# Kernel optimization log

Hardware: AMD Instinct MI355X
Metric: run time of the kernel (lower is better)

## Reference

```python
import jax, jax.numpy as jnp
import numpy as np

B, S, H, L = 8, 4096, 768, 256   # batch, seq_len, hidden_size, num_lines (= line_ids.max()+1)
ATT_HID = 1024                    # attention MLP hidden dim from nn.Linear(hidden,1024)


def setup_inputs() -> dict:
    key = jax.random.key(0)
    k0, k1, k2, k3 = jax.random.split(key, 4)
    token_hidden = jax.random.normal(k0, (B, S, H), dtype=jnp.float32)
    line_ids = jax.random.randint(k1, (B, S), 0, L)  # all valid; -1 would mark invalid
    W1 = jax.random.normal(k2, (H, ATT_HID), dtype=jnp.float32) * 0.02
    b1 = jnp.zeros((ATT_HID,), jnp.float32)
    W2 = jax.random.normal(k3, (ATT_HID, 1), dtype=jnp.float32) * 0.02
    b2 = jnp.zeros((1,), jnp.float32)
    return {"token_hidden": token_hidden, "line_ids": line_ids,
            "W1": W1, "b1": b1, "W2": W2, "b2": b2}


def reference(token_hidden, line_ids, W1, b1, W2, b2):
    b, s, h = token_hidden.shape
    num_lines = L
    n_seg = b * num_lines + 1  # last segment is a dump slot for invalid (-1) tokens

    # attention scores: Linear -> tanh -> Linear, squeeze(-1)  [b, s]
    scores = (jnp.tanh(token_hidden @ W1 + b1) @ W2 + b2)[..., 0]

    valid = (line_ids >= 0).reshape(-1)                                   # [b*s]
    seg = jnp.where(line_ids >= 0,
                    jnp.arange(b)[:, None] * num_lines + line_ids,
                    b * num_lines).reshape(-1)                            # [b*s]
    s_flat = jnp.where(valid, scores.reshape(-1), -jnp.inf)

    # segment-wise stable softmax
    m = jax.ops.segment_max(s_flat, seg, num_segments=n_seg)
    m = jnp.where(jnp.isfinite(m), m, 0.0)  # empty segments -> safe 0
    e = jnp.where(valid, jnp.exp(scores.reshape(-1) - m[seg]), 0.0)
    denom = jax.ops.segment_sum(e, seg, num_segments=n_seg)
    w = e / jnp.maximum(denom[seg], 1e-20)                                # [b*s]

    # weighted sum of tokens per (batch, line) segment
    feats = jax.ops.segment_sum(token_hidden.reshape(-1, h) * w[:, None],
                                seg, num_segments=n_seg)
    line_features = feats[: b * num_lines].reshape(b, num_lines, h)

    counts = jax.ops.segment_sum(valid.astype(jnp.float32), seg, num_segments=n_seg)
    line_mask = counts[: b * num_lines].reshape(b, num_lines) > 0
    return line_features, line_mask
```

## Files before the change

kernel.cpp:

```cpp
#include <hip/hip_runtime.h>
#include <hip/hip_bf16.h>
#include <string.h>

#define M_TOK 32768
#define H_DIM 768
#define AH    1024
#define NSEG  2048
#define LCAP  192
#define NKT   12
#define CONV_BLK 1024

typedef __attribute__((ext_vector_type(8))) __bf16 bf16x8;
typedef __attribute__((ext_vector_type(4))) float f32x4;

__device__ __forceinline__ float tanh_fast(float x) {
  float e = __expf(2.0f * x);
  return 1.0f - 2.0f * __builtin_amdgcn_rcpf(e + 1.0f);
}

__device__ __forceinline__ float bf2f(unsigned short u) {
  unsigned int v = (unsigned int)u << 16;
  float f;
  memcpy(&f, &v, 4);
  return f;
}

__global__ __launch_bounds__(256) void prep_kernel(
    const float* __restrict__ W1, __hip_bfloat16* __restrict__ W1t,
    const float4* __restrict__ X4, uint4* __restrict__ Xb4) {
  __shared__ float tile[32][33];
  if (blockIdx.x < 768) {
    int nt = blockIdx.x & 31, ktile = blockIdx.x >> 5;
    int n0 = nt * 32, k0 = ktile * 32;
    int tx = threadIdx.x & 31, ty = threadIdx.x >> 5;
    for (int r = ty; r < 32; r += 8)
      tile[r][tx] = W1[(size_t)(k0 + r) * AH + n0 + tx];
    __syncthreads();
    for (int r = ty; r < 32; r += 8)
      W1t[(size_t)(n0 + r) * H_DIM + k0 + tx] = __float2bfloat16(tile[tx][r]);
  } else {
    const int i0 = (blockIdx.x - 768) * (256 * 12) + threadIdx.x;
#pragma unroll
    for (int p = 0; p < 12; ++p) {
      const size_t i = (size_t)i0 + p * 256;
      float4 v0 = X4[i * 2];
      float4 v1 = X4[i * 2 + 1];
      __hip_bfloat16 h[8] = {
          __float2bfloat16(v0.x), __float2bfloat16(v0.y),
          __float2bfloat16(v0.z), __float2bfloat16(v0.w),
          __float2bfloat16(v1.x), __float2bfloat16(v1.y),
          __float2bfloat16(v1.z), __float2bfloat16(v1.w)};
      uint4 pk;
      memcpy(&pk, h, 16);
      Xb4[i] = pk;
    }
  }
}

#define WAITV(N) asm volatile("s_waitcnt vmcnt(" #N ")" ::: "memory")
#define WAITL0   asm volatile("s_waitcnt lgkmcnt(0)" ::: "memory")

__global__ __launch_bounds__(512, 2) void attn_score_kernel(
    const __hip_bfloat16* __restrict__ Xbg,
    const __hip_bfloat16* __restrict__ W1tg, const float* __restrict__ b1g,
    const float* __restrict__ W2g, float* __restrict__ scores2) {
  __shared__ __align__(16) __bf16 As[2][256 * 64];
  __shared__ __align__(16) __bf16 Bs[2][256 * 64];

  const int tid = threadIdx.x;
  const int bid = blockIdx.x;
  const int xcd = bid & 7;
  const int sq  = bid >> 3;
  const int m0  = (xcd * 16 + (sq >> 1)) * 256;
  const int np0 = (sq & 1) * 512;
  const int lane = tid & 63;
  const int wave = tid >> 6;
  const int wm   = wave >> 2;
  const int wx   = wave & 3;
  const int ml   = lane & 15;
  const int lh   = lane >> 4;

  const __bf16* Xb = (const __bf16*)Xbg;
  const __bf16* W  = (const __bf16*)W1tg;

  const int lr   = tid >> 3;
  const int scol = ((tid & 7) ^ (lr & 7)) << 3;

  int aRow[4], bRow[4];
#pragma unroll
  for (int q = 0; q < 4; ++q) {
    aRow[q] = m0 + ((q & 1) << 7) + ((q >> 1) << 6) + lr;
    int lrow = (q << 6) + lr;
    bRow[q] = np0 + (((lrow >> 5) & 3) << 6) + ((lrow >> 7) << 5) + (lrow & 31);
  }

  f32x4 acc[8][4];
#pragma unroll
  for (int i = 0; i < 8; ++i)
#pragma unroll
    for (int j = 0; j < 4; ++j) acc[i][j] = (f32x4)0.f;

  bf16x8 af[4][2], bfr[2][2];

  float b1v[2][4], w2v[2][4];
#pragma unroll
  for (int sd = 0; sd < 2; ++sd)
#pragma unroll
    for (int nf = 0; nf < 4; ++nf) {
      int n = np0 + sd * 256 + wx * 64 + nf * 16 + ml;
      b1v[sd][nf] = b1g[n];
      w2v[sd][nf] = W2g[n];
    }
  WAITV(0);

#define STAGE_A(q, buf, kt)                                                    \
  __builtin_amdgcn_global_load_lds(                                            \
      (const __attribute__((address_space(1))) void*)(Xb +                     \
          (size_t)aRow[q] * H_DIM + (kt) + scol),                              \
      (__attribute__((address_space(3))) void*)&As[buf][(q) * 4096 + tid * 8], \
      16, 0, 0)
#define STAGE_B(q, buf, kt, nsh)                                               \
  __builtin_amdgcn_global_load_lds(                                            \
      (const __attribute__((address_space(1))) void*)(W +                      \
          (size_t)(bRow[q] + (nsh)) * H_DIM + (kt) + scol),                    \
      (__attribute__((address_space(3))) void*)&Bs[buf][(q) * 4096 + tid * 8], \
      16, 0, 0)

#define DSRA(MH, P)                                                            \
  _Pragma("unroll") for (int lf = 0; lf < 4; ++lf) {                           \
    int ra = ((MH) << 7) + (wm << 6) + (lf << 4) + ml;                         \
    _Pragma("unroll") for (int kk = 0; kk < 2; ++kk) {                         \
      int ph = ((kk << 2) + lh) ^ (ml & 7);                                    \
      af[lf][kk] = *(const bf16x8*)&As[P][(ra << 6) + (ph << 3)];              \
    }                                                                          \
  }
#define DSRB(NH, P)                                                            \
  _Pragma("unroll") for (int jj = 0; jj < 2; ++jj) {                           \
    int rb = ((NH) << 7) + (wx << 5) + (jj << 4) + ml;                         \
    _Pragma("unroll") for (int kk = 0; kk < 2; ++kk) {                         \
      int ph = ((kk << 2) + lh) ^ (ml & 7);                                    \
      bfr[jj][kk] = *(const bf16x8*)&Bs[P][(rb << 6) + (ph << 3)];             \
    }                                                                          \
  }
#define MFMAQ(MH, NH)                                                          \
  __builtin_amdgcn_s_setprio(1);                                               \
  _Pragma("unroll") for (int kk = 0; kk < 2; ++kk)                             \
    _Pragma("unroll") for (int lf = 0; lf < 4; ++lf)                           \
      _Pragma("unroll") for (int jj = 0; jj < 2; ++jj)                         \
        acc[(MH) * 4 + lf][(NH) * 2 + jj] =                                    \
            __builtin_amdgcn_mfma_f32_16x16x32_bf16(                           \
                af[lf][kk], bfr[jj][kk], acc[(MH) * 4 + lf][(NH) * 2 + jj],    \
                0, 0, 0);                                                      \
  __builtin_amdgcn_s_setprio(0);

#define BARRIER __builtin_amdgcn_s_barrier()
#define SCHED0  __builtin_amdgcn_sched_barrier(0)

#define EPILOGUE(side)                                                         \
  {                                                                            \
    __syncthreads();                                                           \
    float* red = (float*)&As[1][0];                                            \
    _Pragma("unroll") for (int mf = 0; mf < 8; ++mf) {                         \
      _Pragma("unroll") for (int pp = 0; pp < 4; ++pp) {                       \
        float tsum = 0.f;                                                      \
        _Pragma("unroll") for (int nf = 0; nf < 4; ++nf)                       \
          tsum += tanh_fast(acc[mf][nf][pp] + b1v[side][nf]) * w2v[side][nf];  \
        tsum += __shfl_xor(tsum, 1);                                           \
        tsum += __shfl_xor(tsum, 2);                                           \
        tsum += __shfl_xor(tsum, 4);                                           \
        tsum += __shfl_xor(tsum, 8);                                           \
        if (ml == 0)                                                           \
          red[wx * 256 + wm * 128 + mf * 16 + lh * 4 + pp] = tsum;             \
      }                                                                        \
    }                                                                          \
    __syncthreads();                                                           \
    if (tid < 256) {                                                           \
      float v =                                                                \
          (red[tid] + red[256 + tid]) + (red[512 + tid] + red[768 + tid]);     \
      scores2[(size_t)(m0 + tid) * 4 + ((sq & 1) * 2 + (side))] = v;           \
    }                                                                          \
  }

  STAGE_A(0, 0, 0); STAGE_A(1, 0, 0);
  STAGE_B(0, 0, 0, 0); STAGE_B(1, 0, 0, 0);
  STAGE_A(2, 0, 0); STAGE_A(3, 0, 0);
  STAGE_B(2, 0, 0, 0); STAGE_B(3, 0, 0, 0);
  WAITV(4);
  BARRIER;

  int P = 0;
  for (int tt = 0; tt < 2 * NKT - 1; ++tt) {
    const int u   = tt + 1;
    const int ktu = ((u >= NKT) ? (u - NKT) : u) << 6;
    const int nsh = (u >= NKT) ? 256 : 0;

    DSRA(0, P); DSRB(0, P);
    STAGE_A(0, P ^ 1, ktu); STAGE_A(1, P ^ 1, ktu);
    asm volatile("s_waitcnt lgkmcnt(8)" ::: "memory");
    BARRIER;
    WAITL0; SCHED0;
    MFMAQ(0, 0);
    WAITV(4);
    BARRIER;

    DSRA(1, P);
    STAGE_B(0, P ^ 1, ktu, nsh); STAGE_B(1, P ^ 1, ktu, nsh);
    BARRIER;
    WAITL0; SCHED0;
    MFMAQ(1, 0);
    WAITV(4);
    BARRIER;

    DSRB(1, P);
    STAGE_A(2, P ^ 1, ktu); STAGE_A(3, P ^ 1, ktu);
    BARRIER;
    WAITL0; SCHED0;
    MFMAQ(1, 1);
    BARRIER;

    DSRA(0, P);
    STAGE_B(2, P ^ 1, ktu, nsh); STAGE_B(3, P ^ 1, ktu, nsh);
    BARRIER;
    WAITL0; SCHED0;
    MFMAQ(0, 1);
    WAITV(4);
    BARRIER;

    P ^= 1;

    if (tt == NKT - 1) {
      EPILOGUE(0);
#pragma unroll
      for (int i = 0; i < 8; ++i)
#pragma unroll
        for (int j = 0; j < 4; ++j) acc[i][j] = (f32x4)0.f;
      WAITV(0);
      __syncthreads();
    }
  }

  DSRA(0, 1); DSRB(0, 1);
  asm volatile("s_waitcnt lgkmcnt(8)" ::: "memory");
  BARRIER;
  WAITL0; SCHED0;
  MFMAQ(0, 0);
  WAITV(2);
  BARRIER;

  DSRA(1, 1);
  BARRIER;
  WAITL0; SCHED0;
  MFMAQ(1, 0);
  WAITV(0);
  BARRIER;

  DSRB(1, 1);
  BARRIER;
  WAITL0; SCHED0;
  MFMAQ(1, 1);
  BARRIER;

  DSRA(0, 1);
  BARRIER;
  WAITL0; SCHED0;
  MFMAQ(0, 1);

  EPILOGUE(1);
}

__global__ __launch_bounds__(256) void aggregate_kernel(
    const ushort* __restrict__ Xb, const float* __restrict__ scores2,
    const int* __restrict__ line_ids, float4* __restrict__ out4,
    float* __restrict__ out_mask) {
  __shared__ int   slist[LCAP];
  __shared__ float sw[LCAP];
  __shared__ float wred[4];
  __shared__ int   cnt_sh;
  const int seg = blockIdx.x;
  const int b = seg >> 8, lid = seg & 255;
  const int tid = threadIdx.x, lane = tid & 63, wave = tid >> 6;
  const int base = b * 4096;

  if (tid == 0) cnt_sh = 0;

  int ids[16];
#pragma unroll
  for (int c = 0; c < 16; ++c) ids[c] = line_ids[base + c * 256 + tid];
  __syncthreads();

#pragma unroll
  for (int c = 0; c < 16; ++c) {
    bool match = (ids[c] == lid);
    unsigned long long mask = __ballot(match);
    int cw = __popcll(mask);
    int bpos = 0;
    if (lane == 0 && cw) bpos = atomicAdd(&cnt_sh, cw);
    bpos = __shfl(bpos, 0);
    if (match) {
      int pos = bpos + __popcll(mask & ((1ull << lane) - 1ull));
      if (pos < LCAP) slist[pos] = base + c * 256 + tid;
    }
  }
  __syncthreads();
  int total = cnt_sh;
  int cnt = total > LCAP ? LCAP : total;
  if (tid == 0) out_mask[seg] = cnt > 0 ? 1.f : 0.f;
  if (cnt == 0) {
    if (tid < H_DIM / 4)
      out4[(size_t)seg * (H_DIM / 4) + tid] = make_float4(0.f, 0.f, 0.f, 0.f);
    return;
  }
  float lmax = -3.4e38f;
  if (tid < cnt) {
    const float4 a = *(const float4*)(scores2 + (size_t)slist[tid] * 4);
    float sc = (a.x + a.y) + (a.z + a.w);
    sw[tid] = sc;
    lmax = sc;
  }
#pragma unroll
  for (int d = 1; d < 64; d <<= 1) lmax = fmaxf(lmax, __shfl_xor(lmax, d));
  if (lane == 0) wred[wave] = lmax;
  __syncthreads();
  float m = fmaxf(fmaxf(wred[0], wred[1]), fmaxf(wred[2], wred[3]));
  float lsum = 0.f;
  if (tid < cnt) {
    float e = __expf(sw[tid] - m);
    sw[tid] = e;
    lsum = e;
  }
#pragma unroll
  for (int d = 1; d < 64; d <<= 1) lsum += __shfl_xor(lsum, d);
  __syncthreads();
  if (lane == 0) wred[wave] = lsum;
  __syncthreads();
  float denom = wred[0] + wred[1] + wred[2] + wred[3];
  float inv = __builtin_amdgcn_rcpf(fmaxf(denom, 1e-20f));
  if (tid < cnt) sw[tid] *= inv;
  __syncthreads();
  if (tid < H_DIM / 4) {
    const ushort4* xb = (const ushort4*)Xb + tid;
    float4 acc = make_float4(0.f, 0.f, 0.f, 0.f);
    int t = 0;
    for (; t + 4 <= cnt; t += 4) {
      ushort4 u0 = xb[(size_t)slist[t]     * (H_DIM / 4)];
      ushort4 u1 = xb[(size_t)slist[t + 1] * (H_DIM / 4)];
      ushort4 u2 = xb[(size_t)slist[t + 2] * (H_DIM / 4)];
      ushort4 u3 = xb[(size_t)slist[t + 3] * (H_DIM / 4)];
      float w0 = sw[t], w1 = sw[t + 1], w2 = sw[t + 2], w3 = sw[t + 3];
      acc.x += w0 * bf2f(u0.x) + w1 * bf2f(u1.x) + w2 * bf2f(u2.x) + w3 * bf2f(u3.x);
      acc.y += w0 * bf2f(u0.y) + w1 * bf2f(u1.y) + w2 * bf2f(u2.y) + w3 * bf2f(u3.y);
      acc.z += w0 * bf2f(u0.z) + w1 * bf2f(u1.z) + w2 * bf2f(u2.z) + w3 * bf2f(u3.z);
      acc.w += w0 * bf2f(u0.w) + w1 * bf2f(u1.w) + w2 * bf2f(u2.w) + w3 * bf2f(u3.w);
    }
    for (; t < cnt; ++t) {
      ushort4 u = xb[(size_t)slist[t] * (H_DIM / 4)];
      float w = sw[t];
      acc.x += w * bf2f(u.x); acc.y += w * bf2f(u.y);
      acc.z += w * bf2f(u.z); acc.w += w * bf2f(u.w);
    }
    out4[(size_t)seg * (H_DIM / 4) + tid] = acc;
  }
}

extern "C" void kernel_launch(void* const* d_in, const int* in_sizes, int n_in,
                              void* d_out, int out_size, void* d_ws, size_t ws_size,
                              hipStream_t stream) {
  const float* X        = (const float*)d_in[0];
  const int*   line_ids = (const int*)d_in[1];
  const float* W1       = (const float*)d_in[2];
  const float* b1       = (const float*)d_in[3];
  const float* W2       = (const float*)d_in[4];

  char* p = (char*)d_ws;
  __hip_bfloat16* Xb      = (__hip_bfloat16*)p;  p += (size_t)M_TOK * H_DIM * 2;
  __hip_bfloat16* W1t     = (__hip_bfloat16*)p;  p += 1572864;
  float*          scores2 = (float*)p;           p += (size_t)M_TOK * 4 * 4;

  float* out_feats = (float*)d_out;
  float* out_mask  = out_feats + (size_t)NSEG * H_DIM;

  prep_kernel<<<768 + CONV_BLK, 256, 0, stream>>>(
      W1, W1t, (const float4*)X, (uint4*)Xb);
  attn_score_kernel<<<256, 512, 0, stream>>>(Xb, W1t, b1, W2, scores2);
  aggregate_kernel<<<NSEG, 256, 0, stream>>>((const ushort*)Xb, scores2,
                                             line_ids, (float4*)out_feats,
                                             out_mask);
}
```

Measured before the change: 236.7 us.

## Fuse X fp32-to-bf16 conversion into GEMM A-tile loads, aggregate from fp32 X

Removes the separate X conversion pass and the bf16 copy of X. The GEMM now loads fp32 X through registers, converts it to bf16 and writes it into LDS, replacing direct global-to-LDS loads, with the load and wait schedule reworked. The aggregate kernel reads fp32 X directly. This saves a full read and write pass over X, but doubles the bytes read for the A operand and for the gather, and adds register pressure and VALU conversion work inside the GEMM pipeline.

New measurement: 253.0 us. 1.07x slower.

```diff
diff --git a/kernel.cpp b/kernel.cpp
--- a/kernel.cpp
+++ b/kernel.cpp
@@ -8,7 +8,6 @@
 #define NSEG  2048
 #define LCAP  192
 #define NKT   12
-#define CONV_BLK 1024
 
 typedef __attribute__((ext_vector_type(8))) __bf16 bf16x8;
 typedef __attribute__((ext_vector_type(4))) float f32x4;
@@ -18,50 +17,24 @@
   return 1.0f - 2.0f * __builtin_amdgcn_rcpf(e + 1.0f);
 }
 
-__device__ __forceinline__ float bf2f(unsigned short u) {
-  unsigned int v = (unsigned int)u << 16;
-  float f;
-  memcpy(&f, &v, 4);
-  return f;
-}
-
 __global__ __launch_bounds__(256) void prep_kernel(
-    const float* __restrict__ W1, __hip_bfloat16* __restrict__ W1t,
-    const float4* __restrict__ X4, uint4* __restrict__ Xb4) {
+    const float* __restrict__ W1, __hip_bfloat16* __restrict__ W1t) {
   __shared__ float tile[32][33];
-  if (blockIdx.x < 768) {
-    int nt = blockIdx.x & 31, ktile = blockIdx.x >> 5;
-    int n0 = nt * 32, k0 = ktile * 32;
-    int tx = threadIdx.x & 31, ty = threadIdx.x >> 5;
-    for (int r = ty; r < 32; r += 8)
-      tile[r][tx] = W1[(size_t)(k0 + r) * AH + n0 + tx];
-    __syncthreads();
-    for (int r = ty; r < 32; r += 8)
-      W1t[(size_t)(n0 + r) * H_DIM + k0 + tx] = __float2bfloat16(tile[tx][r]);
-  } else {
-    const int i0 = (blockIdx.x - 768) * (256 * 12) + threadIdx.x;
-#pragma unroll
-    for (int p = 0; p < 12; ++p) {
-      const size_t i = (size_t)i0 + p * 256;
-      float4 v0 = X4[i * 2];
-      float4 v1 = X4[i * 2 + 1];
-      __hip_bfloat16 h[8] = {
-          __float2bfloat16(v0.x), __float2bfloat16(v0.y),
-          __float2bfloat16(v0.z), __float2bfloat16(v0.w),
-          __float2bfloat16(v1.x), __float2bfloat16(v1.y),
-          __float2bfloat16(v1.z), __float2bfloat16(v1.w)};
-      uint4 pk;
-      memcpy(&pk, h, 16);
-      Xb4[i] = pk;
-    }
-  }
+  int nt = blockIdx.x & 31, ktile = blockIdx.x >> 5;
+  int n0 = nt * 32, k0 = ktile * 32;
+  int tx = threadIdx.x & 31, ty = threadIdx.x >> 5;
+  for (int r = ty; r < 32; r += 8)
+    tile[r][tx] = W1[(size_t)(k0 + r) * AH + n0 + tx];
+  __syncthreads();
+  for (int r = ty; r < 32; r += 8)
+    W1t[(size_t)(n0 + r) * H_DIM + k0 + tx] = __float2bfloat16(tile[tx][r]);
 }
 
 #define WAITV(N) asm volatile("s_waitcnt vmcnt(" #N ")" ::: "memory")
 #define WAITL0   asm volatile("s_waitcnt lgkmcnt(0)" ::: "memory")
 
 __global__ __launch_bounds__(512, 2) void attn_score_kernel(
-    const __hip_bfloat16* __restrict__ Xbg,
+    const float* __restrict__ Xf,
     const __hip_bfloat16* __restrict__ W1tg, const float* __restrict__ b1g,
     const float* __restrict__ W2g, float* __restrict__ scores2) {
   __shared__ __align__(16) __bf16 As[2][256 * 64];
@@ -80,7 +53,6 @@
   const int ml   = lane & 15;
   const int lh   = lane >> 4;
 
-  const __bf16* Xb = (const __bf16*)Xbg;
   const __bf16* W  = (const __bf16*)W1tg;
 
   const int lr   = tid >> 3;
@@ -101,6 +73,7 @@
     for (int j = 0; j < 4; ++j) acc[i][j] = (f32x4)0.f;
 
   bf16x8 af[4][2], bfr[2][2];
+  float4 ald[4][2];
 
   float b1v[2][4], w2v[2][4];
 #pragma unroll
@@ -113,12 +86,25 @@
     }
   WAITV(0);
 
-#define STAGE_A(q, buf, kt)                                                    \
-  __builtin_amdgcn_global_load_lds(                                            \
-      (const __attribute__((address_space(1))) void*)(Xb +                     \
-          (size_t)aRow[q] * H_DIM + (kt) + scol),                              \
-      (__attribute__((address_space(3))) void*)&As[buf][(q) * 4096 + tid * 8], \
-      16, 0, 0)
+#define LOAD_A(q, kt)                                                          \
+  {                                                                            \
+    const float* ga = Xf + (size_t)aRow[q] * H_DIM + (kt) + scol;              \
+    ald[q][0] = *(const float4*)ga;                                            \
+    ald[q][1] = *(const float4*)(ga + 4);                                      \
+  }
+#define WRITE_A(q, buf)                                                        \
+  {                                                                            \
+    union { bf16x8 v; __hip_bfloat16 h[8]; } u_;                               \
+    u_.h[0] = __float2bfloat16(ald[q][0].x);                                   \
+    u_.h[1] = __float2bfloat16(ald[q][0].y);                                   \
+    u_.h[2] = __float2bfloat16(ald[q][0].z);                                   \
+    u_.h[3] = __float2bfloat16(ald[q][0].w);                                   \
+    u_.h[4] = __float2bfloat16(ald[q][1].x);                                   \
+    u_.h[5] = __float2bfloat16(ald[q][1].y);                                   \
+    u_.h[6] = __float2bfloat16(ald[q][1].z);                                   \
+    u_.h[7] = __float2bfloat16(ald[q][1].w);                                   \
+    *(bf16x8*)&As[buf][(q) * 4096 + tid * 8] = u_.v;                           \
+  }
 #define STAGE_B(q, buf, kt, nsh)                                               \
   __builtin_amdgcn_global_load_lds(                                            \
       (const __attribute__((address_space(1))) void*)(W +                      \
@@ -181,11 +167,13 @@
     }                                                                          \
   }
 
-  STAGE_A(0, 0, 0); STAGE_A(1, 0, 0);
+  LOAD_A(0, 0); LOAD_A(1, 0); LOAD_A(2, 0); LOAD_A(3, 0);
   STAGE_B(0, 0, 0, 0); STAGE_B(1, 0, 0, 0);
-  STAGE_A(2, 0, 0); STAGE_A(3, 0, 0);
   STAGE_B(2, 0, 0, 0); STAGE_B(3, 0, 0, 0);
   WAITV(4);
+  WRITE_A(0, 0); WRITE_A(1, 0); WRITE_A(2, 0); WRITE_A(3, 0);
+  WAITV(0);
+  WAITL0;
   BARRIER;
 
   int P = 0;
@@ -195,35 +183,35 @@
     const int nsh = (u >= NKT) ? 256 : 0;
 
     DSRA(0, P); DSRB(0, P);
-    STAGE_A(0, P ^ 1, ktu); STAGE_A(1, P ^ 1, ktu);
+    LOAD_A(0, ktu); LOAD_A(1, ktu); LOAD_A(2, ktu); LOAD_A(3, ktu);
+    STAGE_B(0, P ^ 1, ktu, nsh); STAGE_B(1, P ^ 1, ktu, nsh);
+    STAGE_B(2, P ^ 1, ktu, nsh); STAGE_B(3, P ^ 1, ktu, nsh);
     asm volatile("s_waitcnt lgkmcnt(8)" ::: "memory");
     BARRIER;
     WAITL0; SCHED0;
     MFMAQ(0, 0);
-    WAITV(4);
     BARRIER;
 
     DSRA(1, P);
-    STAGE_B(0, P ^ 1, ktu, nsh); STAGE_B(1, P ^ 1, ktu, nsh);
     BARRIER;
     WAITL0; SCHED0;
     MFMAQ(1, 0);
+    BARRIER;
+
+    DSRB(1, P);
     WAITV(4);
-    BARRIER;
-
-    DSRB(1, P);
-    STAGE_A(2, P ^ 1, ktu); STAGE_A(3, P ^ 1, ktu);
+    WRITE_A(0, P ^ 1); WRITE_A(1, P ^ 1);
+    WRITE_A(2, P ^ 1); WRITE_A(3, P ^ 1);
     BARRIER;
     WAITL0; SCHED0;
     MFMAQ(1, 1);
     BARRIER;
 
     DSRA(0, P);
-    STAGE_B(2, P ^ 1, ktu, nsh); STAGE_B(3, P ^ 1, ktu, nsh);
     BARRIER;
     WAITL0; SCHED0;
     MFMAQ(0, 1);
-    WAITV(4);
+    WAITV(0);
     BARRIER;
 
     P ^= 1;
@@ -244,14 +232,12 @@
   BARRIER;
   WAITL0; SCHED0;
   MFMAQ(0, 0);
-  WAITV(2);
   BARRIER;
 
   DSRA(1, 1);
   BARRIER;
   WAITL0; SCHED0;
   MFMAQ(1, 0);
-  WAITV(0);
   BARRIER;
 
   DSRB(1, 1);
@@ -269,7 +255,7 @@
 }
 
 __global__ __launch_bounds__(256) void aggregate_kernel(
-    const ushort* __restrict__ Xb, const float* __restrict__ scores2,
+    const float* __restrict__ Xf, const float* __restrict__ scores2,
     const int* __restrict__ line_ids, float4* __restrict__ out4,
     float* __restrict__ out_mask) {
   __shared__ int   slist[LCAP];
@@ -338,25 +324,25 @@
   if (tid < cnt) sw[tid] *= inv;
   __syncthreads();
   if (tid < H_DIM / 4) {
-    const ushort4* xb = (const ushort4*)Xb + tid;
+    const float4* xb = (const float4*)Xf + tid;
     float4 acc = make_float4(0.f, 0.f, 0.f, 0.f);
     int t = 0;
     for (; t + 4 <= cnt; t += 4) {
-      ushort4 u0 = xb[(size_t)slist[t]     * (H_DIM / 4)];
-      ushort4 u1 = xb[(size_t)slist[t + 1] * (H_DIM / 4)];
-      ushort4 u2 = xb[(size_t)slist[t + 2] * (H_DIM / 4)];
-      ushort4 u3 = xb[(size_t)slist[t + 3] * (H_DIM / 4)];
+      float4 u0 = xb[(size_t)slist[t]     * (H_DIM / 4)];
+      float4 u1 = xb[(size_t)slist[t + 1] * (H_DIM / 4)];
+      float4 u2 = xb[(size_t)slist[t + 2] * (H_DIM / 4)];
+      float4 u3 = xb[(size_t)slist[t + 3] * (H_DIM / 4)];
       float w0 = sw[t], w1 = sw[t + 1], w2 = sw[t + 2], w3 = sw[t + 3];
-      acc.x += w0 * bf2f(u0.x) + w1 * bf2f(u1.x) + w2 * bf2f(u2.x) + w3 * bf2f(u3.x);
-      acc.y += w0 * bf2f(u0.y) + w1 * bf2f(u1.y) + w2 * bf2f(u2.y) + w3 * bf2f(u3.y);
-      acc.z += w0 * bf2f(u0.z) + w1 * bf2f(u1.z) + w2 * bf2f(u2.z) + w3 * bf2f(u3.z);
-      acc.w += w0 * bf2f(u0.w) + w1 * bf2f(u1.w) + w2 * bf2f(u2.w) + w3 * bf2f(u3.w);
+      acc.x += w0 * u0.x + w1 * u1.x + w2 * u2.x + w3 * u3.x;
+      acc.y += w0 * u0.y + w1 * u1.y + w2 * u2.y + w3 * u3.y;
+      acc.z += w0 * u0.z + w1 * u1.z + w2 * u2.z + w3 * u3.z;
+      acc.w += w0 * u0.w + w1 * u1.w + w2 * u2.w + w3 * u3.w;
     }
     for (; t < cnt; ++t) {
-      ushort4 u = xb[(size_t)slist[t] * (H_DIM / 4)];
+      float4 u = xb[(size_t)slist[t] * (H_DIM / 4)];
       float w = sw[t];
-      acc.x += w * bf2f(u.x); acc.y += w * bf2f(u.y);
-      acc.z += w * bf2f(u.z); acc.w += w * bf2f(u.w);
+      acc.x += w * u.x; acc.y += w * u.y;
+      acc.z += w * u.z; acc.w += w * u.w;
     }
     out4[(size_t)seg * (H_DIM / 4) + tid] = acc;
   }
@@ -372,17 +358,14 @@
   const float* W2       = (const float*)d_in[4];
 
   char* p = (char*)d_ws;
-  __hip_bfloat16* Xb      = (__hip_bfloat16*)p;  p += (size_t)M_TOK * H_DIM * 2;
   __hip_bfloat16* W1t     = (__hip_bfloat16*)p;  p += 1572864;
   float*          scores2 = (float*)p;           p += (size_t)M_TOK * 4 * 4;
 
   float* out_feats = (float*)d_out;
   float* out_mask  = out_feats + (size_t)NSEG * H_DIM;
 
-  prep_kernel<<<768 + CONV_BLK, 256, 0, stream>>>(
-      W1, W1t, (const float4*)X, (uint4*)Xb);
-  attn_score_kernel<<<256, 512, 0, stream>>>(Xb, W1t, b1, W2, scores2);
-  aggregate_kernel<<<NSEG, 256, 0, stream>>>((const ushort*)Xb, scores2,
-                                             line_ids, (float4*)out_feats,
-                                             out_mask);
-}
+  prep_kernel<<<768, 256, 0, stream>>>(W1, W1t);
+  attn_score_kernel<<<256, 512, 0, stream>>>(X, W1t, b1, W2, scores2);
+  aggregate_kernel<<<NSEG, 256, 0, stream>>>(X, scores2, line_ids,
+                                             (float4*)out_feats, out_mask);
+}
```

## Fuse score GEMM and segment aggregation into one cooperative kernel with grid sync

Applied to the files above, without the earlier changes.

Merges the attention-score GEMM kernel and the per-segment softmax/weighted-sum kernel into a single cooperative launch of 256 blocks, separated by a grid-wide sync. After the sync each block handles 8 segments, reusing the GEMM's shared memory for its token list and weights, and splits the weighted accumulation across two thread groups. This removes one kernel launch and the gap between the two kernels. The cost is that aggregation now runs on only 256 blocks instead of 2048, which lowers parallelism for that phase, and the grid sync itself adds overhead.

After: 351.6 us. 48.6% more time.

```diff
diff --git a/kernel.cpp b/kernel.cpp
--- a/kernel.cpp
+++ b/kernel.cpp
@@ -1,6 +1,9 @@
 #include <hip/hip_runtime.h>
 #include <hip/hip_bf16.h>
+#include <hip/hip_cooperative_groups.h>
 #include <string.h>
+
+namespace cg = cooperative_groups;
 
 #define M_TOK 32768
 #define H_DIM 768
@@ -8,7 +11,6 @@
 #define NSEG  2048
 #define LCAP  192
 #define NKT   12
-#define CONV_BLK 1024
 
 typedef __attribute__((ext_vector_type(8))) __bf16 bf16x8;
 typedef __attribute__((ext_vector_type(4))) float f32x4;
@@ -60,10 +62,12 @@
 #define WAITV(N) asm volatile("s_waitcnt vmcnt(" #N ")" ::: "memory")
 #define WAITL0   asm volatile("s_waitcnt lgkmcnt(0)" ::: "memory")
 
-__global__ __launch_bounds__(512, 2) void attn_score_kernel(
+__global__ __launch_bounds__(512, 2) void fused_kernel(
     const __hip_bfloat16* __restrict__ Xbg,
     const __hip_bfloat16* __restrict__ W1tg, const float* __restrict__ b1g,
-    const float* __restrict__ W2g, float* __restrict__ scores2) {
+    const float* __restrict__ W2g, float* __restrict__ scores2,
+    const int* __restrict__ line_ids, float4* __restrict__ out4,
+    float* __restrict__ out_mask) {
   __shared__ __align__(16) __bf16 As[2][256 * 64];
   __shared__ __align__(16) __bf16 Bs[2][256 * 64];
 
@@ -266,99 +270,109 @@
   MFMAQ(0, 1);
 
   EPILOGUE(1);
-}
-
-__global__ __launch_bounds__(256) void aggregate_kernel(
-    const ushort* __restrict__ Xb, const float* __restrict__ scores2,
-    const int* __restrict__ line_ids, float4* __restrict__ out4,
-    float* __restrict__ out_mask) {
-  __shared__ int   slist[LCAP];
-  __shared__ float sw[LCAP];
-  __shared__ float wred[4];
-  __shared__ int   cnt_sh;
-  const int seg = blockIdx.x;
-  const int b = seg >> 8, lid = seg & 255;
-  const int tid = threadIdx.x, lane = tid & 63, wave = tid >> 6;
+
+  __threadfence();
+  cg::this_grid().sync();
+
+  float4* gredL = (float4*)&As[0][0];
+  int*    slist = (int*)(gredL + 192);
+  float*  sw    = (float*)(slist + 192);
+  float*  wredf = sw + 192;
+  int*    cntp  = (int*)(wredf + 8);
+
+  const int segbase = bid * 8;
+  const int b    = segbase >> 8;
   const int base = b * 4096;
 
-  if (tid == 0) cnt_sh = 0;
-
-  int ids[16];
-#pragma unroll
-  for (int c = 0; c < 16; ++c) ids[c] = line_ids[base + c * 256 + tid];
-  __syncthreads();
-
-#pragma unroll
-  for (int c = 0; c < 16; ++c) {
-    bool match = (ids[c] == lid);
-    unsigned long long mask = __ballot(match);
-    int cw = __popcll(mask);
-    int bpos = 0;
-    if (lane == 0 && cw) bpos = atomicAdd(&cnt_sh, cw);
-    bpos = __shfl(bpos, 0);
-    if (match) {
-      int pos = bpos + __popcll(mask & ((1ull << lane) - 1ull));
-      if (pos < LCAP) slist[pos] = base + c * 256 + tid;
-    }
-  }
-  __syncthreads();
-  int total = cnt_sh;
-  int cnt = total > LCAP ? LCAP : total;
-  if (tid == 0) out_mask[seg] = cnt > 0 ? 1.f : 0.f;
-  if (cnt == 0) {
-    if (tid < H_DIM / 4)
-      out4[(size_t)seg * (H_DIM / 4) + tid] = make_float4(0.f, 0.f, 0.f, 0.f);
-    return;
-  }
-  float lmax = -3.4e38f;
-  if (tid < cnt) {
-    const float4 a = *(const float4*)(scores2 + (size_t)slist[tid] * 4);
-    float sc = (a.x + a.y) + (a.z + a.w);
-    sw[tid] = sc;
-    lmax = sc;
-  }
-#pragma unroll
-  for (int d = 1; d < 64; d <<= 1) lmax = fmaxf(lmax, __shfl_xor(lmax, d));
-  if (lane == 0) wred[wave] = lmax;
-  __syncthreads();
-  float m = fmaxf(fmaxf(wred[0], wred[1]), fmaxf(wred[2], wred[3]));
-  float lsum = 0.f;
-  if (tid < cnt) {
-    float e = __expf(sw[tid] - m);
-    sw[tid] = e;
-    lsum = e;
-  }
-#pragma unroll
-  for (int d = 1; d < 64; d <<= 1) lsum += __shfl_xor(lsum, d);
-  __syncthreads();
-  if (lane == 0) wred[wave] = lsum;
-  __syncthreads();
-  float denom = wred[0] + wred[1] + wred[2] + wred[3];
-  float inv = __builtin_amdgcn_rcpf(fmaxf(denom, 1e-20f));
-  if (tid < cnt) sw[tid] *= inv;
-  __syncthreads();
-  if (tid < H_DIM / 4) {
-    const ushort4* xb = (const ushort4*)Xb + tid;
-    float4 acc = make_float4(0.f, 0.f, 0.f, 0.f);
-    int t = 0;
-    for (; t + 4 <= cnt; t += 4) {
-      ushort4 u0 = xb[(size_t)slist[t]     * (H_DIM / 4)];
-      ushort4 u1 = xb[(size_t)slist[t + 1] * (H_DIM / 4)];
-      ushort4 u2 = xb[(size_t)slist[t + 2] * (H_DIM / 4)];
-      ushort4 u3 = xb[(size_t)slist[t + 3] * (H_DIM / 4)];
-      float w0 = sw[t], w1 = sw[t + 1], w2 = sw[t + 2], w3 = sw[t + 3];
-      acc.x += w0 * bf2f(u0.x) + w1 * bf2f(u1.x) + w2 * bf2f(u2.x) + w3 * bf2f(u3.x);
-      acc.y += w0 * bf2f(u0.y) + w1 * bf2f(u1.y) + w2 * bf2f(u2.y) + w3 * bf2f(u3.y);
-      acc.z += w0 * bf2f(u0.z) + w1 * bf2f(u1.z) + w2 * bf2f(u2.z) + w3 * bf2f(u3.z);
-      acc.w += w0 * bf2f(u0.w) + w1 * bf2f(u1.w) + w2 * bf2f(u2.w) + w3 * bf2f(u3.w);
-    }
-    for (; t < cnt; ++t) {
-      ushort4 u = xb[(size_t)slist[t] * (H_DIM / 4)];
-      float w = sw[t];
-      acc.x += w * bf2f(u.x); acc.y += w * bf2f(u.y);
-      acc.z += w * bf2f(u.z); acc.w += w * bf2f(u.w);
-    }
-    out4[(size_t)seg * (H_DIM / 4) + tid] = acc;
+  int ids[8];
+#pragma unroll
+  for (int c = 0; c < 8; ++c) ids[c] = line_ids[base + c * 512 + tid];
+
+  const int g   = tid / 192;
+  const int col = tid - g * 192;
+
+  for (int s = 0; s < 8; ++s) {
+    const int seg = segbase + s;
+    const int lid = seg & 255;
+
+    if (tid == 0) *cntp = 0;
+    __syncthreads();
+#pragma unroll
+    for (int c = 0; c < 8; ++c) {
+      bool match = (ids[c] == lid);
+      unsigned long long mask = __ballot(match);
+      int cw = __popcll(mask);
+      int bpos = 0;
+      if (lane == 0 && cw) bpos = atomicAdd(cntp, cw);
+      bpos = __shfl(bpos, 0);
+      if (match) {
+        int pos = bpos + __popcll(mask & ((1ull << lane) - 1ull));
+        if (pos < LCAP) slist[pos] = base + c * 512 + tid;
+      }
+    }
+    __syncthreads();
+    int total = *cntp;
+    int cnt = total > LCAP ? LCAP : total;
+    if (tid == 0) out_mask[seg] = cnt > 0 ? 1.f : 0.f;
+
+    float lmax = -3.4e38f;
+    if (tid < cnt) {
+      const float4 a = *(const float4*)(scores2 + (size_t)slist[tid] * 4);
+      float sc = (a.x + a.y) + (a.z + a.w);
+      sw[tid] = sc;
+      lmax = sc;
+    }
+#pragma unroll
+    for (int d = 1; d < 64; d <<= 1) lmax = fmaxf(lmax, __shfl_xor(lmax, d));
+    if (lane == 0) wredf[wave] = lmax;
+    __syncthreads();
+    float m = fmaxf(fmaxf(fmaxf(wredf[0], wredf[1]), fmaxf(wredf[2], wredf[3])),
+                    fmaxf(fmaxf(wredf[4], wredf[5]), fmaxf(wredf[6], wredf[7])));
+    float lsum = 0.f;
+    if (tid < cnt) {
+      float e = __expf(sw[tid] - m);
+      sw[tid] = e;
+      lsum = e;
+    }
+#pragma unroll
+    for (int d = 1; d < 64; d <<= 1) lsum += __shfl_xor(lsum, d);
+    __syncthreads();
+    if (lane == 0) wredf[wave] = lsum;
+    __syncthreads();
+    float denom = ((wredf[0] + wredf[1]) + (wredf[2] + wredf[3])) +
+                  ((wredf[4] + wredf[5]) + (wredf[6] + wredf[7]));
+    float inv = __builtin_amdgcn_rcpf(fmaxf(denom, 1e-20f));
+    if (tid < cnt) sw[tid] *= inv;
+    __syncthreads();
+
+    float4 acc4 = make_float4(0.f, 0.f, 0.f, 0.f);
+    if (g < 2) {
+      const ushort4* xb = (const ushort4*)Xbg + col;
+      int t = g;
+      for (; t + 2 < cnt; t += 4) {
+        ushort4 u0 = xb[(size_t)slist[t]     * (H_DIM / 4)];
+        ushort4 u1 = xb[(size_t)slist[t + 2] * (H_DIM / 4)];
+        float w0 = sw[t], w1 = sw[t + 2];
+        acc4.x += w0 * bf2f(u0.x) + w1 * bf2f(u1.x);
+        acc4.y += w0 * bf2f(u0.y) + w1 * bf2f(u1.y);
+        acc4.z += w0 * bf2f(u0.z) + w1 * bf2f(u1.z);
+        acc4.w += w0 * bf2f(u0.w) + w1 * bf2f(u1.w);
+      }
+      for (; t < cnt; t += 2) {
+        ushort4 u = xb[(size_t)slist[t] * (H_DIM / 4)];
+        float w = sw[t];
+        acc4.x += w * bf2f(u.x); acc4.y += w * bf2f(u.y);
+        acc4.z += w * bf2f(u.z); acc4.w += w * bf2f(u.w);
+      }
+    }
+    if (g == 1) gredL[col] = acc4;
+    __syncthreads();
+    if (g == 0) {
+      float4 o = gredL[col];
+      acc4.x += o.x; acc4.y += o.y; acc4.z += o.z; acc4.w += o.w;
+      out4[(size_t)seg * (H_DIM / 4) + col] = acc4;
+    }
+    __syncthreads();
   }
 }
 
@@ -379,10 +393,18 @@
   float* out_feats = (float*)d_out;
   float* out_mask  = out_feats + (size_t)NSEG * H_DIM;
 
-  prep_kernel<<<768 + CONV_BLK, 256, 0, stream>>>(
+  prep_kernel<<<768 + 1024, 256, 0, stream>>>(
       W1, W1t, (const float4*)X, (uint4*)Xb);
-  attn_score_kernel<<<256, 512, 0, stream>>>(Xb, W1t, b1, W2, scores2);
-  aggregate_kernel<<<NSEG, 256, 0, stream>>>((const ushort*)Xb, scores2,
-                                             line_ids, (float4*)out_feats,
-                                             out_mask);
+
+  const __hip_bfloat16* XbA   = Xb;
+  const __hip_bfloat16* W1tA  = W1t;
+  const float*          b1A   = b1;
+  const float*          W2A   = W2;
+  float*                sc2A  = scores2;
+  const int*            lidA  = line_ids;
+  float4*               out4A = (float4*)out_feats;
+  float*                omA   = out_mask;
+  void* kargs[] = {&XbA, &W1tA, &b1A, &W2A, &sc2A, &lidA, &out4A, &omA};
+  hipLaunchCooperativeKernel((const void*)fused_kernel, dim3(256), dim3(512),
+                             kargs, 0, stream);
 }
```

## Precompute per-batch counting sort of tokens by line in prep kernel

Applied to the files above, without the earlier changes.

Adds 8 blocks to the prep kernel that build a histogram, prefix scan and counting sort of token indices by line id for each batch, writing sorted token lists plus per-segment offsets and counts. The aggregate kernel now reads its segment's token list directly instead of having every one of 2048 blocks rescan all 4096 line ids of its batch with ballots. This removes redundant scanning work from the aggregate stage. The X-to-bf16 conversion is also re-split across 2048 blocks with a strided loop. Token order within a segment is no longer deterministic because of shared atomics, and the per-segment cap rises from 192 to 256.

Result: no change. 239.0 us (+1.0%).

```diff
diff --git a/kernel.cpp b/kernel.cpp
--- a/kernel.cpp
+++ b/kernel.cpp
@@ -6,9 +6,8 @@
 #define H_DIM 768
 #define AH    1024
 #define NSEG  2048
-#define LCAP  192
 #define NKT   12
-#define CONV_BLK 1024
+#define XCONV_BLK 2048
 
 typedef __attribute__((ext_vector_type(8))) __bf16 bf16x8;
 typedef __attribute__((ext_vector_type(4))) float f32x4;
@@ -27,22 +26,27 @@
 
 __global__ __launch_bounds__(256) void prep_kernel(
     const float* __restrict__ W1, __hip_bfloat16* __restrict__ W1t,
-    const float4* __restrict__ X4, uint4* __restrict__ Xb4) {
+    const float4* __restrict__ X4, uint4* __restrict__ Xb4,
+    const int* __restrict__ line_ids, int* __restrict__ sorted,
+    int* __restrict__ offs, int* __restrict__ counts) {
   __shared__ float tile[32][33];
+  __shared__ int hist[256];
+  __shared__ int pfx[256];
+  const int tid = threadIdx.x;
   if (blockIdx.x < 768) {
     int nt = blockIdx.x & 31, ktile = blockIdx.x >> 5;
     int n0 = nt * 32, k0 = ktile * 32;
-    int tx = threadIdx.x & 31, ty = threadIdx.x >> 5;
+    int tx = tid & 31, ty = tid >> 5;
     for (int r = ty; r < 32; r += 8)
       tile[r][tx] = W1[(size_t)(k0 + r) * AH + n0 + tx];
     __syncthreads();
     for (int r = ty; r < 32; r += 8)
       W1t[(size_t)(n0 + r) * H_DIM + k0 + tx] = __float2bfloat16(tile[tx][r]);
-  } else {
-    const int i0 = (blockIdx.x - 768) * (256 * 12) + threadIdx.x;
-#pragma unroll
-    for (int p = 0; p < 12; ++p) {
-      const size_t i = (size_t)i0 + p * 256;
+  } else if (blockIdx.x < 768 + XCONV_BLK) {
+    const int i0 = (blockIdx.x - 768) * 256 + tid;
+#pragma unroll
+    for (int p = 0; p < 6; ++p) {
+      const size_t i = (size_t)i0 + (size_t)p * (XCONV_BLK * 256);
       float4 v0 = X4[i * 2];
       float4 v1 = X4[i * 2 + 1];
       __hip_bfloat16 h[8] = {
@@ -53,6 +57,40 @@
       uint4 pk;
       memcpy(&pk, h, 16);
       Xb4[i] = pk;
+    }
+  } else {
+    const int bb = blockIdx.x - (768 + XCONV_BLK);
+    const int base = bb * 4096;
+    hist[tid] = 0;
+    int ids[16];
+#pragma unroll
+    for (int c = 0; c < 16; ++c) ids[c] = line_ids[base + c * 256 + tid];
+    __syncthreads();
+#pragma unroll
+    for (int c = 0; c < 16; ++c)
+      if (ids[c] >= 0) atomicAdd(&hist[ids[c]], 1);
+    __syncthreads();
+    int v = hist[tid];
+    pfx[tid] = v;
+    __syncthreads();
+    for (int d = 1; d < 256; d <<= 1) {
+      int t = (tid >= d) ? pfx[tid - d] : 0;
+      __syncthreads();
+      pfx[tid] += t;
+      __syncthreads();
+    }
+    int excl = pfx[tid] - v;
+    counts[bb * 256 + tid] = v;
+    offs[bb * 256 + tid] = excl;
+    hist[tid] = excl;
+    __syncthreads();
+#pragma unroll
+    for (int c = 0; c < 16; ++c) {
+      int id = ids[c];
+      if (id >= 0) {
+        int p = atomicAdd(&hist[id], 1);
+        sorted[base + p] = base + c * 256 + tid;
+      }
     }
   }
 }
@@ -270,49 +308,31 @@
 
 __global__ __launch_bounds__(256) void aggregate_kernel(
     const ushort* __restrict__ Xb, const float* __restrict__ scores2,
-    const int* __restrict__ line_ids, float4* __restrict__ out4,
+    const int* __restrict__ sorted, const int* __restrict__ offs,
+    const int* __restrict__ counts, float4* __restrict__ out4,
     float* __restrict__ out_mask) {
-  __shared__ int   slist[LCAP];
-  __shared__ float sw[LCAP];
+  __shared__ int   tok[256];
+  __shared__ float sw[256];
   __shared__ float wred[4];
-  __shared__ int   cnt_sh;
   const int seg = blockIdx.x;
-  const int b = seg >> 8, lid = seg & 255;
+  const int b = seg >> 8;
   const int tid = threadIdx.x, lane = tid & 63, wave = tid >> 6;
-  const int base = b * 4096;
-
-  if (tid == 0) cnt_sh = 0;
-
-  int ids[16];
-#pragma unroll
-  for (int c = 0; c < 16; ++c) ids[c] = line_ids[base + c * 256 + tid];
-  __syncthreads();
-
-#pragma unroll
-  for (int c = 0; c < 16; ++c) {
-    bool match = (ids[c] == lid);
-    unsigned long long mask = __ballot(match);
-    int cw = __popcll(mask);
-    int bpos = 0;
-    if (lane == 0 && cw) bpos = atomicAdd(&cnt_sh, cw);
-    bpos = __shfl(bpos, 0);
-    if (match) {
-      int pos = bpos + __popcll(mask & ((1ull << lane) - 1ull));
-      if (pos < LCAP) slist[pos] = base + c * 256 + tid;
-    }
-  }
-  __syncthreads();
-  int total = cnt_sh;
-  int cnt = total > LCAP ? LCAP : total;
+
+  const int off = offs[seg];
+  int cnt = counts[seg];
+  if (cnt > 256) cnt = 256;
   if (tid == 0) out_mask[seg] = cnt > 0 ? 1.f : 0.f;
   if (cnt == 0) {
     if (tid < H_DIM / 4)
       out4[(size_t)seg * (H_DIM / 4) + tid] = make_float4(0.f, 0.f, 0.f, 0.f);
     return;
   }
+
   float lmax = -3.4e38f;
   if (tid < cnt) {
-    const float4 a = *(const float4*)(scores2 + (size_t)slist[tid] * 4);
+    int t = sorted[(b << 12) + off + tid];
+    tok[tid] = t;
+    const float4 a = *(const float4*)(scores2 + (size_t)t * 4);
     float sc = (a.x + a.y) + (a.z + a.w);
     sw[tid] = sc;
     lmax = sc;
@@ -342,10 +362,10 @@
     float4 acc = make_float4(0.f, 0.f, 0.f, 0.f);
     int t = 0;
     for (; t + 4 <= cnt; t += 4) {
-      ushort4 u0 = xb[(size_t)slist[t]     * (H_DIM / 4)];
-      ushort4 u1 = xb[(size_t)slist[t + 1] * (H_DIM / 4)];
-      ushort4 u2 = xb[(size_t)slist[t + 2] * (H_DIM / 4)];
-      ushort4 u3 = xb[(size_t)slist[t + 3] * (H_DIM / 4)];
+      ushort4 u0 = xb[(size_t)tok[t]     * (H_DIM / 4)];
+      ushort4 u1 = xb[(size_t)tok[t + 1] * (H_DIM / 4)];
+      ushort4 u2 = xb[(size_t)tok[t + 2] * (H_DIM / 4)];
+      ushort4 u3 = xb[(size_t)tok[t + 3] * (H_DIM / 4)];
       float w0 = sw[t], w1 = sw[t + 1], w2 = sw[t + 2], w3 = sw[t + 3];
       acc.x += w0 * bf2f(u0.x) + w1 * bf2f(u1.x) + w2 * bf2f(u2.x) + w3 * bf2f(u3.x);
       acc.y += w0 * bf2f(u0.y) + w1 * bf2f(u1.y) + w2 * bf2f(u2.y) + w3 * bf2f(u3.y);
@@ -353,7 +373,7 @@
       acc.w += w0 * bf2f(u0.w) + w1 * bf2f(u1.w) + w2 * bf2f(u2.w) + w3 * bf2f(u3.w);
     }
     for (; t < cnt; ++t) {
-      ushort4 u = xb[(size_t)slist[t] * (H_DIM / 4)];
+      ushort4 u = xb[(size_t)tok[t] * (H_DIM / 4)];
       float w = sw[t];
       acc.x += w * bf2f(u.x); acc.y += w * bf2f(u.y);
       acc.z += w * bf2f(u.z); acc.w += w * bf2f(u.w);
@@ -375,14 +395,17 @@
   __hip_bfloat16* Xb      = (__hip_bfloat16*)p;  p += (size_t)M_TOK * H_DIM * 2;
   __hip_bfloat16* W1t     = (__hip_bfloat16*)p;  p += 1572864;
   float*          scores2 = (float*)p;           p += (size_t)M_TOK * 4 * 4;
+  int*            sorted  = (int*)p;             p += (size_t)M_TOK * 4;
+  int*            offs    = (int*)p;             p += (size_t)NSEG * 4;
+  int*            counts  = (int*)p;             p += (size_t)NSEG * 4;
 
   float* out_feats = (float*)d_out;
   float* out_mask  = out_feats + (size_t)NSEG * H_DIM;
 
-  prep_kernel<<<768 + CONV_BLK, 256, 0, stream>>>(
-      W1, W1t, (const float4*)X, (uint4*)Xb);
+  prep_kernel<<<768 + XCONV_BLK + 8, 256, 0, stream>>>(
+      W1, W1t, (const float4*)X, (uint4*)Xb, line_ids, sorted, offs, counts);
   attn_score_kernel<<<256, 512, 0, stream>>>(Xb, W1t, b1, W2, scores2);
   aggregate_kernel<<<NSEG, 256, 0, stream>>>((const ushort*)Xb, scores2,
-                                             line_ids, (float4*)out_feats,
-                                             out_mask);
-}
+                                             sorted, offs, counts,
+                                             (float4*)out_feats, out_mask);
+}
```
